# Performance work log

Hardware: AMD Instinct MI355X
Metric: run time of the kernel (lower is better)

The kernel has to match this reference:

```python
import jax, jax.numpy as jnp
import numpy as np

B, S, D, H = 4, 2048, 1024, 16
HD = D // H  # 64


def setup_inputs() -> dict:
    key = jax.random.key(0)
    ks = jax.random.split(key, 8)
    s = 0.02
    return {
        "inp_values": jax.random.normal(ks[0], (B, S, D), jnp.float32),
        "inp_keys": jax.random.normal(ks[1], (B, S, D), jnp.float32),
        "inp_queries": jax.random.normal(ks[2], (B, S, D), jnp.float32),
        # per-head projection weights, torch nn.Linear(head_dims, head_dims, bias=False): y = x @ W.T
        "Wv": jax.random.normal(ks[3], (HD, HD), jnp.float32) * s,
        "Wk": jax.random.normal(ks[4], (HD, HD), jnp.float32) * s,
        "Wq": jax.random.normal(ks[5], (HD, HD), jnp.float32) * s,
        # output projection nn.Linear(D, D) with bias
        "Wo": jax.random.normal(ks[6], (D, D), jnp.float32) * s,
        "bo": jax.random.normal(ks[7], (D,), jnp.float32) * s,
    }


def reference(inp_values, inp_keys, inp_queries, Wv, Wk, Wq, Wo, bo):
    b, sq, _ = inp_queries.shape
    sk = inp_values.shape[1]
    v = inp_values.reshape(b, sk, H, HD)
    k = inp_keys.reshape(b, sk, H, HD)
    q = inp_queries.reshape(b, sq, H, HD)
    # per-head linear: x @ W.T
    v = jnp.einsum('bshd,ed->bshe', v, Wv)
    k = jnp.einsum('bshd,ed->bshe', k, Wk)
    q = jnp.einsum('bshd,ed->bshe', q, Wq)
    # scores scaled by 1/sqrt(input_dims) as in the original (not head_dims)
    scores = jnp.einsum('bqhd,bkhd->bhqk', q, k) / jnp.sqrt(jnp.float32(D))
    attn = jax.nn.softmax(scores, axis=-1)  # [B,H,Q,K]
    out = jnp.einsum('bhqk,bkhd->bqhd', attn, v).reshape(b, sq, D)
    return out @ Wo.T + bo
```

## Files before the change

### kernel.cpp

```cpp
#include <hip/hip_runtime.h>
#include <hip/hip_bf16.h>

#define B_ 4
#define S_ 2048
#define D_ 1024
#define H_ 16
#define HD_ 64

typedef __attribute__((ext_vector_type(8))) short bf16x8;
typedef __attribute__((ext_vector_type(4))) float f32x4;

#define MFMA32(a, b, c) __builtin_amdgcn_mfma_f32_16x16x32_bf16(a, b, c, 0, 0, 0)

__device__ __forceinline__ float fast_exp2(float x) {
#if __has_builtin(__builtin_amdgcn_exp2f)
  return __builtin_amdgcn_exp2f(x);
#else
  return exp2f(x);
#endif
}

__device__ __forceinline__ float fast_rcp(float x) {
#if __has_builtin(__builtin_amdgcn_rcpf)
  return __builtin_amdgcn_rcpf(x);
#else
  return 1.0f / x;
#endif
}

__device__ __forceinline__ short f2bf(float x) {
  union { float f; unsigned u; } v; v.f = x;
  unsigned r = (v.u + 0x7fffu + ((v.u >> 16) & 1u)) >> 16;
  return (short)(r & 0xffffu);
}

__device__ __forceinline__ unsigned pack_hi16(float a, float b) {
  union { float f; unsigned u; } ua, ub; ua.f = a; ub.f = b;
  return __builtin_amdgcn_perm(ub.u, ua.u, 0x07060302u);
}

__device__ __forceinline__ void gl_lds16(const short* g, void* l) {
  __builtin_amdgcn_global_load_lds(
      (const __attribute__((address_space(1))) unsigned*)(const void*)g,
      (__attribute__((address_space(3))) unsigned*)l, 16, 0, 0);
}

__global__ __launch_bounds__(256) void wo_convert(const float* __restrict__ Wo,
                                                  short* __restrict__ wob) {
  int i = blockIdx.x * blockDim.x + threadIdx.x;
  const float4* src = (const float4*)Wo + i * 2;
  float4 a = src[0], b = src[1];
  bf16x8 o;
  o[0] = f2bf(a.x); o[1] = f2bf(a.y); o[2] = f2bf(a.z); o[3] = f2bf(a.w);
  o[4] = f2bf(b.x); o[5] = f2bf(b.y); o[6] = f2bf(b.z); o[7] = f2bf(b.w);
  ((bf16x8*)wob)[i] = o;
}

__global__ __launch_bounds__(256) void qkv_proj2(
    const float* __restrict__ inpV, const float* __restrict__ inpK,
    const float* __restrict__ inpQ, const float* __restrict__ Wv,
    const float* __restrict__ Wk, const float* __restrict__ Wq,
    short* __restrict__ vt, short* __restrict__ kp, short* __restrict__ qp) {
  __shared__ bf16x8 xbuf[1024];
  __shared__ bf16x8 wbuf[512];
  int bid = blockIdx.x;
  int t = bid >> 10;
  int bh = (bid >> 4) & 63;
  int st = bid & 15;
  int b = bh >> 4, h = bh & 15;
  int s0 = st * 128;
  int tid = threadIdx.x, wave = tid >> 6, lane = tid & 63;
  int quad = lane >> 4, l15 = lane & 15;
  const float* inp = (t == 0) ? inpV : (t == 1) ? inpK : inpQ;
  const float* W = (t == 0) ? Wv : (t == 1) ? Wk : Wq;
  float wscale = (t == 2) ? (0.03125f * 1.4426950408889634f) : 1.0f;

#pragma unroll
  for (int u = 0; u < 2; ++u) {
    int slot = tid + u * 256;
    int row = slot >> 3, g = slot & 7;
    const float4* wp = (const float4*)(W + row * 64 + g * 8);
    float4 w0 = wp[0], w1 = wp[1];
    bf16x8 o;
    o[0] = f2bf(w0.x * wscale); o[1] = f2bf(w0.y * wscale);
    o[2] = f2bf(w0.z * wscale); o[3] = f2bf(w0.w * wscale);
    o[4] = f2bf(w1.x * wscale); o[5] = f2bf(w1.y * wscale);
    o[6] = f2bf(w1.z * wscale); o[7] = f2bf(w1.w * wscale);
    wbuf[row * 8 + (g ^ (row & 7))] = o;
  }
  const float* xg = inp + (b * S_ + s0) * D_ + h * HD_;
#pragma unroll
  for (int u = 0; u < 4; ++u) {
    int slot = tid + u * 256;
    int row = slot >> 3, g = slot & 7;
    const float4* xp = (const float4*)(xg + row * D_ + g * 8);
    float4 x0 = xp[0], x1 = xp[1];
    bf16x8 o;
    o[0] = f2bf(x0.x); o[1] = f2bf(x0.y); o[2] = f2bf(x0.z); o[3] = f2bf(x0.w);
    o[4] = f2bf(x1.x); o[5] = f2bf(x1.y); o[6] = f2bf(x1.z); o[7] = f2bf(x1.w);
    xbuf[row * 8 + (g ^ (row & 7))] = o;
  }
  __syncthreads();

  if (t == 0) {
    f32x4 acc[4][2];
#pragma unroll
    for (int mt = 0; mt < 4; mt++)
#pragma unroll
      for (int nt = 0; nt < 2; nt++) { acc[mt][nt][0]=0.f; acc[mt][nt][1]=0.f; acc[mt][nt][2]=0.f; acc[mt][nt][3]=0.f; }
#pragma unroll
    for (int ks = 0; ks < 2; ++ks) {
      bf16x8 af[4], bfr[2];
#pragma unroll
      for (int mt = 0; mt < 4; ++mt) {
        int row = mt * 16 + l15;
        af[mt] = wbuf[row * 8 + ((ks * 4 + quad) ^ (row & 7))];
      }
#pragma unroll
      for (int nt = 0; nt < 2; ++nt) {
        int row = wave * 32 + nt * 16 + l15;
        bfr[nt] = xbuf[row * 8 + ((ks * 4 + quad) ^ (row & 7))];
      }
#pragma unroll
      for (int mt = 0; mt < 4; ++mt)
#pragma unroll
        for (int nt = 0; nt < 2; ++nt)
          acc[mt][nt] = MFMA32(af[mt], bfr[nt], acc[mt][nt]);
    }
    short* vb = vt + (bh * 64) * S_ + s0 + wave * 32;
#pragma unroll
    for (int mt = 0; mt < 4; ++mt)
#pragma unroll
      for (int nt = 0; nt < 2; ++nt)
#pragma unroll
        for (int r = 0; r < 4; ++r) {
          int e = mt * 16 + quad * 4 + r;
          int s = nt * 16 + l15;
          vb[e * S_ + s] = f2bf(acc[mt][nt][r]);
        }
  } else {
    f32x4 acc[2][4];
#pragma unroll
    for (int mt = 0; mt < 2; mt++)
#pragma unroll
      for (int nt = 0; nt < 4; nt++) { acc[mt][nt][0]=0.f; acc[mt][nt][1]=0.f; acc[mt][nt][2]=0.f; acc[mt][nt][3]=0.f; }
#pragma unroll
    for (int ks = 0; ks < 2; ++ks) {
      bf16x8 af[2], bfr[4];
#pragma unroll
      for (int mt = 0; mt < 2; ++mt) {
        int row = wave * 32 + mt * 16 + l15;
        af[mt] = xbuf[row * 8 + ((ks * 4 + quad) ^ (row & 7))];
      }
#pragma unroll
      for (int nt = 0; nt < 4; ++nt) {
        int row = nt * 16 + l15;
        bfr[nt] = wbuf[row * 8 + ((ks * 4 + quad) ^ (row & 7))];
      }
#pragma unroll
      for (int mt = 0; mt < 2; ++mt)
#pragma unroll
        for (int nt = 0; nt < 4; ++nt)
          acc[mt][nt] = MFMA32(af[mt], bfr[nt], acc[mt][nt]);
    }
    short* ob = ((t == 1) ? kp : qp) + (bh * S_ + s0 + wave * 32) * 64;
#pragma unroll
    for (int mt = 0; mt < 2; ++mt)
#pragma unroll
      for (int nt = 0; nt < 4; ++nt)
#pragma unroll
        for (int r = 0; r < 4; ++r) {
          int s = mt * 16 + quad * 4 + r;
          int e = nt * 16 + l15;
          ob[s * 64 + e] = f2bf(acc[mt][nt][r]);
        }
  }
}

__global__ __launch_bounds__(128, 4) void attention(
    const short* __restrict__ qp, const short* __restrict__ kp,
    const short* __restrict__ vt, short* __restrict__ ao) {
  __shared__ bf16x8 kbuf[2][256];
  __shared__ bf16x8 vbuf[2][256];
  int bid = blockIdx.x;
  int qt = bid >> 6;
  int bh = bid & 63;
  int tid = threadIdx.x, wave = tid >> 6, lane = tid & 63;
  int quad = lane >> 4, l15 = lane & 15;

  const short* qb = qp + (bh * S_ + qt * 64 + wave * 32 + l15) * 64;
  bf16x8 bq[2][2];
  bq[0][0] = *(const bf16x8*)(qb + quad * 8);
  bq[0][1] = *(const bf16x8*)(qb + 32 + quad * 8);
  bq[1][0] = *(const bf16x8*)(qb + 1024 + quad * 8);
  bq[1][1] = *(const bf16x8*)(qb + 1024 + 32 + quad * 8);

  const f32x4 fzero = {0.f, 0.f, 0.f, 0.f};
  f32x4 o[2][4];
#pragma unroll
  for (int g = 0; g < 2; g++)
#pragma unroll
    for (int dt = 0; dt < 4; dt++) o[g][dt] = fzero;
  f32x4 lacc[2];
  lacc[0] = fzero; lacc[1] = fzero;

  short one_bf = (short)0x3F80;
  bf16x8 ones8;
#pragma unroll
  for (int j = 0; j < 8; ++j) ones8[j] = (l15 == 0) ? one_bf : (short)0;

  const short* kg = kp + bh * S_ * 64;
  const short* vg = vt + bh * 64 * S_;

  int krow0 = tid >> 3, kg0 = (tid & 7) ^ (krow0 & 7);
  int krow1 = (tid + 128) >> 3, kg1 = (tid & 7) ^ (krow1 & 7);
  const short* kA = kg + krow0 * 64 + kg0 * 8;
  const short* kB = kg + krow1 * 64 + kg1 * 8;
  int vrow0 = tid >> 2, vg0 = (tid & 3) ^ (vrow0 & 3);
  int vrow1 = (tid + 128) >> 2, vg1 = (tid & 3) ^ (vrow1 & 3);
  const short* vA = vg + vrow0 * S_ + vg0 * 8;
  const short* vB = vg + vrow1 * S_ + vg1 * 8;

  gl_lds16(kA, &kbuf[0][tid]);
  gl_lds16(kB, &kbuf[0][tid + 128]);
  gl_lds16(vA, &vbuf[0][tid]);
  gl_lds16(vB, &vbuf[0][tid + 128]);

  int krp0 = ((l15 >> 2) << 3) + (l15 & 3);

  int p = 0;
  for (int kt = 0; kt < 64; ++kt) {
    __syncthreads();
    int ktn = (kt + 1) & 63;
    gl_lds16(kA + ktn * 2048, &kbuf[p ^ 1][tid]);
    gl_lds16(kB + ktn * 2048, &kbuf[p ^ 1][tid + 128]);
    gl_lds16(vA + ktn * 32, &vbuf[p ^ 1][tid]);
    gl_lds16(vB + ktn * 32, &vbuf[p ^ 1][tid + 128]);

    union Frag { unsigned u[4]; bf16x8 v; };
    Frag pa0, pa1;
#pragma unroll
    for (int nt = 0; nt < 2; ++nt) {
      int krow = krp0 + nt * 4;
      bf16x8 ak0 = kbuf[p][krow * 8 + ((0 + quad) ^ (krow & 7))];
      bf16x8 ak1 = kbuf[p][krow * 8 + ((4 + quad) ^ (krow & 7))];
      f32x4 c0 = MFMA32(ak0, bq[0][0], fzero);
      f32x4 c1 = MFMA32(ak0, bq[1][0], fzero);
      c0 = MFMA32(ak1, bq[0][1], c0);
      c1 = MFMA32(ak1, bq[1][1], c1);
      float e00 = fast_exp2(c0[0]), e01 = fast_exp2(c0[1]);
      float e02 = fast_exp2(c0[2]), e03 = fast_exp2(c0[3]);
      float e10 = fast_exp2(c1[0]), e11 = fast_exp2(c1[1]);
      float e12 = fast_exp2(c1[2]), e13 = fast_exp2(c1[3]);
      pa0.u[nt * 2 + 0] = pack_hi16(e00, e01);
      pa0.u[nt * 2 + 1] = pack_hi16(e02, e03);
      pa1.u[nt * 2 + 0] = pack_hi16(e10, e11);
      pa1.u[nt * 2 + 1] = pack_hi16(e12, e13);
    }
    lacc[0] = MFMA32(pa0.v, ones8, lacc[0]);
    lacc[1] = MFMA32(pa1.v, ones8, lacc[1]);
#pragma unroll
    for (int dt = 0; dt < 4; ++dt) {
      int d = dt * 16 + l15;
      bf16x8 bv = vbuf[p][d * 4 + (quad ^ (d & 3))];
      o[0][dt] = MFMA32(pa0.v, bv, o[0][dt]);
      o[1][dt] = MFMA32(pa1.v, bv, o[1][dt]);
    }
    p ^= 1;
  }

  int b = bh >> 4, h = bh & 15;
#pragma unroll
  for (int g = 0; g < 2; ++g) {
    float inv[4];
#pragma unroll
    for (int r = 0; r < 4; ++r) {
      float ls = __shfl(lacc[g][r], lane & 48, 64);
      inv[r] = fast_rcp(ls);
    }
#pragma unroll
    for (int dt = 0; dt < 4; ++dt)
#pragma unroll
      for (int r = 0; r < 4; ++r) {
        int srow = qt * 64 + wave * 32 + g * 16 + quad * 4 + r;
        ao[(b * S_ + srow) * D_ + h * 64 + dt * 16 + l15] =
            f2bf(o[g][dt][r] * inv[r]);
      }
  }
}

__global__ __launch_bounds__(256) void outproj(const short* __restrict__ A,
                                               const short* __restrict__ Bw,
                                               const float* __restrict__ bo,
                                               float* __restrict__ out) {
  __shared__ bf16x8 sa[2][1024];
  __shared__ bf16x8 sb[2][1024];
  int bid = blockIdx.x;
  int m0 = (bid >> 3) * 128, n0 = (bid & 7) * 128;
  int tid = threadIdx.x, wave = tid >> 6, lane = tid & 63;
  int quad = lane >> 4, l15 = lane & 15;
  int wm = (wave >> 1) * 64, wn = (wave & 1) * 64;
  f32x4 acc[4][4];
#pragma unroll
  for (int mt = 0; mt < 4; mt++)
#pragma unroll
    for (int nt = 0; nt < 4; nt++) { acc[mt][nt][0]=0.f; acc[mt][nt][1]=0.f; acc[mt][nt][2]=0.f; acc[mt][nt][3]=0.f; }

  const short* asrc[4];
  const short* bsrc[4];
#pragma unroll
  for (int u = 0; u < 4; ++u) {
    int slot = tid + u * 256;
    int row = slot >> 3, g = (slot & 7) ^ (row & 7);
    asrc[u] = A + (m0 + row) * 1024 + g * 8;
    bsrc[u] = Bw + (n0 + row) * 1024 + g * 8;
  }
#pragma unroll
  for (int u = 0; u < 4; ++u) {
    gl_lds16(asrc[u], &sa[0][tid + u * 256]);
    gl_lds16(bsrc[u], &sb[0][tid + u * 256]);
  }

  int p = 0;
  for (int k0 = 0; k0 < 1024; k0 += 64) {
    __syncthreads();
    int kn = (k0 + 64) & 1023;
#pragma unroll
    for (int u = 0; u < 4; ++u) {
      gl_lds16(asrc[u] + kn, &sa[p ^ 1][tid + u * 256]);
      gl_lds16(bsrc[u] + kn, &sb[p ^ 1][tid + u * 256]);
    }
#pragma unroll
    for (int ks = 0; ks < 2; ++ks) {
      bf16x8 af[4], bf[4];
#pragma unroll
      for (int mt = 0; mt < 4; ++mt) {
        int row = wm + mt * 16 + l15;
        af[mt] = sa[p][row * 8 + ((ks * 4 + quad) ^ (row & 7))];
      }
#pragma unroll
      for (int nt = 0; nt < 4; ++nt) {
        int row = wn + nt * 16 + l15;
        bf[nt] = sb[p][row * 8 + ((ks * 4 + quad) ^ (row & 7))];
      }
#pragma unroll
      for (int mt = 0; mt < 4; ++mt)
#pragma unroll
        for (int nt = 0; nt < 4; ++nt)
          acc[mt][nt] = MFMA32(af[mt], bf[nt], acc[mt][nt]);
    }
    p ^= 1;
  }
#pragma unroll
  for (int nt = 0; nt < 4; ++nt) {
    int n = n0 + wn + nt * 16 + l15;
    float bov = bo[n];
#pragma unroll
    for (int mt = 0; mt < 4; ++mt)
#pragma unroll
      for (int r = 0; r < 4; r++) {
        int m = m0 + wm + mt * 16 + quad * 4 + r;
        out[m * 1024 + n] = acc[mt][nt][r] + bov;
      }
  }
}

extern "C" void kernel_launch(void* const* d_in, const int* in_sizes, int n_in,
                              void* d_out, int out_size, void* d_ws,
                              size_t ws_size, hipStream_t stream) {
  const float* inpV = (const float*)d_in[0];
  const float* inpK = (const float*)d_in[1];
  const float* inpQ = (const float*)d_in[2];
  const float* Wv = (const float*)d_in[3];
  const float* Wk = (const float*)d_in[4];
  const float* Wq = (const float*)d_in[5];
  const float* Wo = (const float*)d_in[6];
  const float* bo = (const float*)d_in[7];
  float* out = (float*)d_out;

  char* ws = (char*)d_ws;
  short* vt = (short*)(ws);
  short* kp = (short*)(ws + (16u << 20));
  short* qp = (short*)(ws + (32u << 20));
  short* ao = (short*)(ws + (48u << 20));
  short* wob = (short*)(ws + (64u << 20));

  wo_convert<<<dim3(512), dim3(256), 0, stream>>>(Wo, wob);
  qkv_proj2<<<dim3(3072), dim3(256), 0, stream>>>(inpV, inpK, inpQ, Wv, Wk, Wq,
                                                  vt, kp, qp);
  attention<<<dim3(2048), dim3(128), 0, stream>>>(qp, kp, vt, ao);
  outproj<<<dim3(512), dim3(256), 0, stream>>>(ao, wob, bo, out);
}
```

Before: 269.2 us.

## Fold Wo conversion into QKV kernel and restructure attention inner loop

Merges the separate Wo-to-bf16 conversion kernel into the QKV projection launch as an extra 512 blocks, removing one kernel launch. In the attention kernel, changes the K tile LDS swizzle to a new pattern and precomputes the LDS fragment slot indices outside the loop. It also unrolls the key loop by two with constant buffer parity and raises wave priority around the MFMA block with s_setprio. The aim is fewer launches, fewer LDS bank conflicts and less per-iteration index arithmetic, at the cost of extra register use and a more complex loop.

```diff
diff --git a/kernel.cpp b/kernel.cpp
--- a/kernel.cpp
+++ b/kernel.cpp
@@ -11,6 +11,8 @@
 typedef __attribute__((ext_vector_type(4))) float f32x4;
 
 #define MFMA32(a, b, c) __builtin_amdgcn_mfma_f32_16x16x32_bf16(a, b, c, 0, 0, 0)
+
+#define KSWZ(r) ((((r) & 3)) ^ ((((r) >> 3) & 1) << 2))
 
 __device__ __forceinline__ float fast_exp2(float x) {
 #if __has_builtin(__builtin_amdgcn_exp2f)
@@ -45,32 +47,34 @@
       (__attribute__((address_space(3))) unsigned*)l, 16, 0, 0);
 }
 
-__global__ __launch_bounds__(256) void wo_convert(const float* __restrict__ Wo,
-                                                  short* __restrict__ wob) {
-  int i = blockIdx.x * blockDim.x + threadIdx.x;
-  const float4* src = (const float4*)Wo + i * 2;
-  float4 a = src[0], b = src[1];
-  bf16x8 o;
-  o[0] = f2bf(a.x); o[1] = f2bf(a.y); o[2] = f2bf(a.z); o[3] = f2bf(a.w);
-  o[4] = f2bf(b.x); o[5] = f2bf(b.y); o[6] = f2bf(b.z); o[7] = f2bf(b.w);
-  ((bf16x8*)wob)[i] = o;
-}
-
 __global__ __launch_bounds__(256) void qkv_proj2(
     const float* __restrict__ inpV, const float* __restrict__ inpK,
     const float* __restrict__ inpQ, const float* __restrict__ Wv,
     const float* __restrict__ Wk, const float* __restrict__ Wq,
+    const float* __restrict__ Wo, short* __restrict__ wob,
     short* __restrict__ vt, short* __restrict__ kp, short* __restrict__ qp) {
   __shared__ bf16x8 xbuf[1024];
   __shared__ bf16x8 wbuf[512];
   int bid = blockIdx.x;
   int t = bid >> 10;
+  int tid = threadIdx.x, wave = tid >> 6, lane = tid & 63;
+  int quad = lane >> 4, l15 = lane & 15;
+
+  if (t == 3) {
+    int i = (bid & 511) * 256 + tid;
+    const float4* src = (const float4*)Wo + i * 2;
+    float4 a = src[0], b = src[1];
+    bf16x8 o;
+    o[0] = f2bf(a.x); o[1] = f2bf(a.y); o[2] = f2bf(a.z); o[3] = f2bf(a.w);
+    o[4] = f2bf(b.x); o[5] = f2bf(b.y); o[6] = f2bf(b.z); o[7] = f2bf(b.w);
+    ((bf16x8*)wob)[i] = o;
+    return;
+  }
+
   int bh = (bid >> 4) & 63;
   int st = bid & 15;
   int b = bh >> 4, h = bh & 15;
   int s0 = st * 128;
-  int tid = threadIdx.x, wave = tid >> 6, lane = tid & 63;
-  int quad = lane >> 4, l15 = lane & 15;
   const float* inp = (t == 0) ? inpV : (t == 1) ? inpK : inpQ;
   const float* W = (t == 0) ? Wv : (t == 1) ? Wk : Wq;
   float wscale = (t == 2) ? (0.03125f * 1.4426950408889634f) : 1.0f;
@@ -212,8 +216,8 @@
   const short* kg = kp + bh * S_ * 64;
   const short* vg = vt + bh * 64 * S_;
 
-  int krow0 = tid >> 3, kg0 = (tid & 7) ^ (krow0 & 7);
-  int krow1 = (tid + 128) >> 3, kg1 = (tid & 7) ^ (krow1 & 7);
+  int krow0 = tid >> 3, kg0 = (tid & 7) ^ KSWZ(krow0);
+  int krow1 = (tid + 128) >> 3, kg1 = (tid & 7) ^ KSWZ(krow1);
   const short* kA = kg + krow0 * 64 + kg0 * 8;
   const short* kB = kg + krow1 * 64 + kg1 * 8;
   int vrow0 = tid >> 2, vg0 = (tid & 3) ^ (vrow0 & 3);
@@ -228,46 +232,62 @@
 
   int krp0 = ((l15 >> 2) << 3) + (l15 & 3);
 
-  int p = 0;
-  for (int kt = 0; kt < 64; ++kt) {
-    __syncthreads();
-    int ktn = (kt + 1) & 63;
-    gl_lds16(kA + ktn * 2048, &kbuf[p ^ 1][tid]);
-    gl_lds16(kB + ktn * 2048, &kbuf[p ^ 1][tid + 128]);
-    gl_lds16(vA + ktn * 32, &vbuf[p ^ 1][tid]);
-    gl_lds16(vB + ktn * 32, &vbuf[p ^ 1][tid + 128]);
-
-    union Frag { unsigned u[4]; bf16x8 v; };
-    Frag pa0, pa1;
-#pragma unroll
-    for (int nt = 0; nt < 2; ++nt) {
-      int krow = krp0 + nt * 4;
-      bf16x8 ak0 = kbuf[p][krow * 8 + ((0 + quad) ^ (krow & 7))];
-      bf16x8 ak1 = kbuf[p][krow * 8 + ((4 + quad) ^ (krow & 7))];
-      f32x4 c0 = MFMA32(ak0, bq[0][0], fzero);
-      f32x4 c1 = MFMA32(ak0, bq[1][0], fzero);
-      c0 = MFMA32(ak1, bq[0][1], c0);
-      c1 = MFMA32(ak1, bq[1][1], c1);
-      float e00 = fast_exp2(c0[0]), e01 = fast_exp2(c0[1]);
-      float e02 = fast_exp2(c0[2]), e03 = fast_exp2(c0[3]);
-      float e10 = fast_exp2(c1[0]), e11 = fast_exp2(c1[1]);
-      float e12 = fast_exp2(c1[2]), e13 = fast_exp2(c1[3]);
-      pa0.u[nt * 2 + 0] = pack_hi16(e00, e01);
-      pa0.u[nt * 2 + 1] = pack_hi16(e02, e03);
-      pa1.u[nt * 2 + 0] = pack_hi16(e10, e11);
-      pa1.u[nt * 2 + 1] = pack_hi16(e12, e13);
-    }
-    lacc[0] = MFMA32(pa0.v, ones8, lacc[0]);
-    lacc[1] = MFMA32(pa1.v, ones8, lacc[1]);
-#pragma unroll
-    for (int dt = 0; dt < 4; ++dt) {
-      int d = dt * 16 + l15;
-      bf16x8 bv = vbuf[p][d * 4 + (quad ^ (d & 3))];
-      o[0][dt] = MFMA32(pa0.v, bv, o[0][dt]);
-      o[1][dt] = MFMA32(pa1.v, bv, o[1][dt]);
-    }
-    p ^= 1;
-  }
+  int aslot0[2], aslot1[2], vslot[4];
+#pragma unroll
+  for (int nt = 0; nt < 2; ++nt) {
+    int krow = krp0 + nt * 4;
+    aslot0[nt] = krow * 8 + ((0 + quad) ^ KSWZ(krow));
+    aslot1[nt] = krow * 8 + ((4 + quad) ^ KSWZ(krow));
+  }
+#pragma unroll
+  for (int dt = 0; dt < 4; ++dt) {
+    int d = dt * 16 + l15;
+    vslot[dt] = d * 4 + (quad ^ (d & 3));
+  }
+
+#define ATTN_BODY(P, T)                                                     \
+  do {                                                                      \
+    __syncthreads();                                                        \
+    int ktn = ((T) + 1) & 63;                                               \
+    gl_lds16(kA + ktn * 2048, &kbuf[(P) ^ 1][tid]);                         \
+    gl_lds16(kB + ktn * 2048, &kbuf[(P) ^ 1][tid + 128]);                   \
+    gl_lds16(vA + ktn * 32, &vbuf[(P) ^ 1][tid]);                           \
+    gl_lds16(vB + ktn * 32, &vbuf[(P) ^ 1][tid + 128]);                     \
+    union Frag { unsigned u[4]; bf16x8 v; } pa0, pa1;                       \
+    _Pragma("unroll")                                                       \
+    for (int nt = 0; nt < 2; ++nt) {                                        \
+      bf16x8 ak0 = kbuf[(P)][aslot0[nt]];                                   \
+      bf16x8 ak1 = kbuf[(P)][aslot1[nt]];                                   \
+      f32x4 c0 = MFMA32(ak0, bq[0][0], fzero);                              \
+      f32x4 c1 = MFMA32(ak0, bq[1][0], fzero);                              \
+      c0 = MFMA32(ak1, bq[0][1], c0);                                       \
+      c1 = MFMA32(ak1, bq[1][1], c1);                                       \
+      float e00 = fast_exp2(c0[0]), e01 = fast_exp2(c0[1]);                 \
+      float e02 = fast_exp2(c0[2]), e03 = fast_exp2(c0[3]);                 \
+      float e10 = fast_exp2(c1[0]), e11 = fast_exp2(c1[1]);                 \
+      float e12 = fast_exp2(c1[2]), e13 = fast_exp2(c1[3]);                 \
+      pa0.u[nt * 2 + 0] = pack_hi16(e00, e01);                              \
+      pa0.u[nt * 2 + 1] = pack_hi16(e02, e03);                              \
+      pa1.u[nt * 2 + 0] = pack_hi16(e10, e11);                              \
+      pa1.u[nt * 2 + 1] = pack_hi16(e12, e13);                              \
+    }                                                                       \
+    __builtin_amdgcn_s_setprio(1);                                          \
+    lacc[0] = MFMA32(pa0.v, ones8, lacc[0]);                                \
+    lacc[1] = MFMA32(pa1.v, ones8, lacc[1]);                                \
+    _Pragma("unroll")                                                       \
+    for (int dt = 0; dt < 4; ++dt) {                                        \
+      bf16x8 bv = vbuf[(P)][vslot[dt]];                                     \
+      o[0][dt] = MFMA32(pa0.v, bv, o[0][dt]);                               \
+      o[1][dt] = MFMA32(pa1.v, bv, o[1][dt]);                               \
+    }                                                                       \
+    __builtin_amdgcn_s_setprio(0);                                          \
+  } while (0)
+
+  for (int kt = 0; kt < 64; kt += 2) {
+    ATTN_BODY(0, kt);
+    ATTN_BODY(1, kt + 1);
+  }
+#undef ATTN_BODY
 
   int b = bh >> 4, h = bh & 15;
 #pragma unroll
@@ -385,9 +405,8 @@
   short* ao = (short*)(ws + (48u << 20));
   short* wob = (short*)(ws + (64u << 20));
 
-  wo_convert<<<dim3(512), dim3(256), 0, stream>>>(Wo, wob);
-  qkv_proj2<<<dim3(3072), dim3(256), 0, stream>>>(inpV, inpK, inpQ, Wv, Wk, Wq,
-                                                  vt, kp, qp);
+  qkv_proj2<<<dim3(3584), dim3(256), 0, stream>>>(inpV, inpK, inpQ, Wv, Wk, Wq,
+                                                  Wo, wob, vt, kp, qp);
   attention<<<dim3(2048), dim3(128), 0, stream>>>(qp, kp, vt, ao);
   outproj<<<dim3(512), dim3(256), 0, stream>>>(ao, wob, bo, out);
 }
```

Result: no change. 265.0 us (-1.6%).
